# Optimization experiments

Measured on AMD Instinct MI355X. Metric: run time of the kernel, lower is better.

The kernel has to match this reference:

```python
import jax, jax.numpy as jnp
import numpy as np

N_HEADS, N_LEVELS, N_POINTS, D_MODEL = 8, 4, 4, 256
HEAD_DIM = D_MODEL // N_HEADS
SHAPES = [(96, 96), (48, 48), (24, 24), (12, 12)]


def setup_inputs() -> dict:
    key = jax.random.key(0)
    ks = jax.random.split(key, 9)
    shapes_np = np.asarray(SHAPES, dtype=np.int32)
    lengths = shapes_np[:, 0] * shapes_np[:, 1]
    Len = int(lengths.sum())  # 12240
    B = 1
    level_start = np.concatenate([[0], np.cumsum(lengths)[:-1]]).astype(np.int32)
    return {
        "query": jax.random.normal(ks[0], (B, Len, D_MODEL), jnp.float32),
        "reference_points": jax.random.uniform(ks[1], (B, Len, 2), jnp.float32),
        "input_flatten": jax.random.normal(ks[2], (B, Len, D_MODEL), jnp.float32),
        "spatial_shapes": jnp.asarray(shapes_np),
        "level_start_index": jnp.asarray(level_start),
        "W_off": jax.random.normal(ks[3], (D_MODEL, N_HEADS * N_LEVELS * N_POINTS * 2), jnp.float32) * 0.01,
        "b_off": jax.random.normal(ks[4], (N_HEADS * N_LEVELS * N_POINTS * 2,), jnp.float32) * 0.01,
        "W_attn": jax.random.normal(ks[5], (D_MODEL, N_HEADS * N_LEVELS * N_POINTS), jnp.float32) * 0.02,
        "b_attn": jnp.zeros((N_HEADS * N_LEVELS * N_POINTS,), jnp.float32),
        "W_out": jax.random.normal(ks[6], (D_MODEL, D_MODEL), jnp.float32) * 0.02,
        "b_out": jnp.zeros((D_MODEL,), jnp.float32),
    }


def _bilinear_gather(feat, x, y, H, W):
    """feat: [B,nH,H*W,D]; x,y: [B,nH,S] pixel coords. Zero padding, align_corners=False."""
    x0 = jnp.floor(x)
    y0 = jnp.floor(y)
    wx1 = x - x0
    wy1 = y - y0
    wx0 = 1.0 - wx1
    wy0 = 1.0 - wy1
    x0i = x0.astype(jnp.int32)
    y0i = y0.astype(jnp.int32)

    def corner(ix, iy):
        valid = (ix >= 0) & (ix < W) & (iy >= 0) & (iy < H)
        idx = jnp.clip(iy, 0, H - 1) * W + jnp.clip(ix, 0, W - 1)
        g = jnp.take_along_axis(feat, idx[..., None], axis=2)  # [B,nH,S,D]
        return g * valid[..., None].astype(feat.dtype)

    return (corner(x0i, y0i) * (wx0 * wy0)[..., None]
            + corner(x0i + 1, y0i) * (wx1 * wy0)[..., None]
            + corner(x0i, y0i + 1) * (wx0 * wy1)[..., None]
            + corner(x0i + 1, y0i + 1) * (wx1 * wy1)[..., None])


def _ms_deform_core(value, shapes_np, loc, attn):
    """value: [B,Len_in,nH,D]; loc: [B,LQ,nH,nL,nP,2]; attn: [B,LQ,nH,nL,nP]."""
    B, LQ = loc.shape[0], loc.shape[1]
    lengths = [int(h) * int(w) for h, w in shapes_np]
    starts = np.concatenate([[0], np.cumsum(lengths)])
    out = jnp.zeros((B, N_HEADS, LQ, HEAD_DIM), value.dtype)
    for lvl, (H, W) in enumerate(shapes_np):
        H, W = int(H), int(W)
        feat = value[:, starts[lvl]:starts[lvl + 1]].transpose(0, 2, 1, 3)  # [B,nH,HW,D]
        l = loc[:, :, :, lvl]  # [B,LQ,nH,nP,2]
        x = (l[..., 0] * W - 0.5).transpose(0, 2, 1, 3).reshape(B, N_HEADS, LQ * N_POINTS)
        y = (l[..., 1] * H - 0.5).transpose(0, 2, 1, 3).reshape(B, N_HEADS, LQ * N_POINTS)
        samp = _bilinear_gather(feat, x, y, H, W).reshape(B, N_HEADS, LQ, N_POINTS, HEAD_DIM)
        w = attn[:, :, :, lvl].transpose(0, 2, 1, 3)  # [B,nH,LQ,nP]
        out = out + (samp * w[..., None]).sum(axis=3)
    return out.transpose(0, 2, 1, 3).reshape(B, LQ, N_HEADS * HEAD_DIM)


def reference(query, reference_points, input_flatten, spatial_shapes, level_start_index,
              W_off, b_off, W_attn, b_attn, W_out, b_out):
    B, LQ, C = query.shape
    shapes_np = np.asarray(spatial_shapes)  # static per-level (H,W)
    off = (query @ W_off + b_off).reshape(B, LQ, N_HEADS, N_LEVELS, N_POINTS, 2)
    attn = jax.nn.softmax((query @ W_attn + b_attn).reshape(B, LQ, N_HEADS, N_LEVELS * N_POINTS), axis=-1)
    attn = attn.reshape(B, LQ, N_HEADS, N_LEVELS, N_POINTS)
    # offset_normalizer = (W, H) per level
    norm = jnp.asarray(np.stack([shapes_np[:, 1], shapes_np[:, 0]], -1), dtype=query.dtype)
    loc = reference_points[:, :, None, None, None, :] + off / norm[None, None, None, :, None, :]
    value = input_flatten.reshape(B, -1, N_HEADS, HEAD_DIM)
    out = _ms_deform_core(value, shapes_np, loc, attn)
    return out @ W_out + b_out
```

## Files before the change

kernel.cpp:

```cpp
#include <hip/hip_runtime.h>
#include <hip/hip_bf16.h>
#include <math.h>

constexpr int D_MODEL  = 256;
constexpr int N_HEADS  = 8;

typedef __attribute__((ext_vector_type(8))) short bf16x8;
typedef __attribute__((ext_vector_type(4))) float f32x4;
typedef __attribute__((ext_vector_type(2))) float f32x2;

__device__ __forceinline__ void gld_lds16(const void* gsrc, void* ldst) {
    __builtin_amdgcn_global_load_lds(
        (const __attribute__((address_space(1))) unsigned int*)gsrc,
        (__attribute__((address_space(3))) unsigned int*)ldst, 16, 0, 0);
}

__global__ __launch_bounds__(256) void convert_kernel(
    const float* __restrict__ q,
    const float* __restrict__ Woff,
    const float* __restrict__ Wattn,
    const float* __restrict__ Wout,
    const float* __restrict__ value,
    __hip_bfloat16* __restrict__ qbf,
    __hip_bfloat16* __restrict__ wt,
    __hip_bfloat16* __restrict__ vt,
    int M, int Lv)
{
    int t = blockIdx.x * 256 + threadIdx.x;
    int nq4 = M * 64;
    if (t < nq4) {
        float4 v = reinterpret_cast<const float4*>(q)[t];
        union { __hip_bfloat16 h[4]; ushort4 u; } cv;
        cv.h[0] = __float2bfloat16(v.x);
        cv.h[1] = __float2bfloat16(v.y);
        cv.h[2] = __float2bfloat16(v.z);
        cv.h[3] = __float2bfloat16(v.w);
        reinterpret_cast<ushort4*>(qbf)[t] = cv.u;
        return;
    }
    int t2 = t - nq4;
    if (t2 < 640 * 256) {
        int c = t2 >> 8, k = t2 & 255;
        float val = (c < 256) ? Woff[k * 256 + c]
                  : (c < 384) ? Wattn[k * 128 + (c - 256)]
                              : Wout[k * 256 + (c - 384)];
        wt[c * 256 + k] = __float2bfloat16(val);
        return;
    }
    int t3 = t2 - 640 * 256;
    if (t3 < Lv * 64) {
        int pix = t3 >> 6;
        int c4  = (t3 & 63) * 4;
        int h   = c4 >> 5, d = c4 & 31;
        float4 v = reinterpret_cast<const float4*>(value)[t3];
        union { __hip_bfloat16 h4[4]; ushort4 u; } cv;
        cv.h4[0] = __float2bfloat16(v.x);
        cv.h4[1] = __float2bfloat16(v.y);
        cv.h4[2] = __float2bfloat16(v.z);
        cv.h4[3] = __float2bfloat16(v.w);
        *reinterpret_cast<ushort4*>(vt + (size_t)h * Lv * 32 + (size_t)pix * 32 + d) = cv.u;
    }
}

template <int EPI>
__global__ __launch_bounds__(256) void gemm_mfma(
    const __hip_bfloat16* __restrict__ Abf,
    const __hip_bfloat16* __restrict__ Wt,
    int wrow0,
    const float* __restrict__ ba,
    const float* __restrict__ bb,
    const float* __restrict__ refpts,
    float* __restrict__ out0,
    float* __restrict__ out1,
    int M)
{
    __shared__ __align__(16) char smem[128 * 68 * 4];
    char*  A_lds = smem;
    char*  B_lds = smem + 16384;
    float* C_lds = (float*)smem;

    const int tid = threadIdx.x;
    const int w = tid >> 6, l = tid & 63;
    const int m0 = blockIdx.y * 128;
    const int n0 = blockIdx.x * 64;

    const char* Asrc = (const char*)Abf;
    const char* Wsrc = (const char*)(Wt + (size_t)(wrow0 + n0) * 256);

    f32x4 acc[2][4] = {};

    const int lr8 = l >> 3, l7 = l & 7;

    for (int k0 = 0; k0 < 512; k0 += 128) {
#pragma unroll
        for (int i = 0; i < 4; ++i) {
            int chunk = (w << 2) + i;
            int row = (chunk << 3) + lr8;
            int m = m0 + row; m = m < M ? m : (M - 1);
            gld_lds16(Asrc + (size_t)m * 512 + k0 + ((l7 ^ (row & 7)) << 4),
                      A_lds + (chunk << 10));
        }
#pragma unroll
        for (int i = 0; i < 2; ++i) {
            int chunk = (w << 1) + i;
            int row = (chunk << 3) + lr8;
            gld_lds16(Wsrc + (size_t)row * 512 + k0 + ((l7 ^ (row & 7)) << 4),
                      B_lds + (chunk << 10));
        }
        __syncthreads();

#pragma unroll
        for (int kk = 0; kk < 2; ++kk) {
            bf16x8 av[2], bv[4];
#pragma unroll
            for (int mf = 0; mf < 2; ++mf) {
                int arow = (w << 5) + (mf << 4) + (l & 15);
                int acb = ((kk << 6) + ((l >> 4) << 4)) ^ ((arow & 7) << 4);
                av[mf] = *(const bf16x8*)(A_lds + arow * 128 + acb);
            }
#pragma unroll
            for (int nf = 0; nf < 4; ++nf) {
                int brow = (nf << 4) + (l & 15);
                int bcb = ((kk << 6) + ((l >> 4) << 4)) ^ ((brow & 7) << 4);
                bv[nf] = *(const bf16x8*)(B_lds + brow * 128 + bcb);
            }
#pragma unroll
            for (int mf = 0; mf < 2; ++mf)
#pragma unroll
                for (int nf = 0; nf < 4; ++nf)
                    acc[mf][nf] = __builtin_amdgcn_mfma_f32_16x16x32_bf16(
                        av[mf], bv[nf], acc[mf][nf], 0, 0, 0);
        }
        __syncthreads();
    }

#pragma unroll
    for (int mf = 0; mf < 2; ++mf)
#pragma unroll
        for (int nf = 0; nf < 4; ++nf) {
            int col = (nf << 4) + (l & 15);
            int rbase = (w << 5) + (mf << 4) + ((l >> 4) << 2);
#pragma unroll
            for (int j = 0; j < 4; ++j)
                C_lds[(rbase + j) * 68 + col] = acc[mf][nf][j];
        }
    __syncthreads();

    if (EPI == 0 || n0 < 256) {
#pragma unroll
        for (int r2 = 0; r2 < 2; ++r2) {
            int row = (r2 << 6) + (tid >> 2);
            int q = m0 + row;
            if (q >= M) continue;
            float rx = 0.f, ry = 0.f;
            if (EPI == 1) { rx = refpts[q * 2]; ry = refpts[q * 2 + 1]; }
#pragma unroll
            for (int g = 0; g < 4; ++g) {
                int col = ((tid & 3) << 4) + (g << 2);
                float4 v  = *(float4*)&C_lds[row * 68 + col];
                float4 b4 = *(const float4*)&ba[n0 + col];
                if (EPI == 0) {
                    v.x += b4.x; v.y += b4.y; v.z += b4.z; v.w += b4.w;
                } else {
                    int c = n0 + col;
                    float rn = 1.0f / (float)(96 >> ((c >> 3) & 3));
                    v.x = rx + (v.x + b4.x) * rn;
                    v.y = ry + (v.y + b4.y) * rn;
                    v.z = rx + (v.z + b4.z) * rn;
                    v.w = ry + (v.w + b4.w) * rn;
                }
                *(float4*)&out0[(size_t)q * 256 + n0 + col] = v;
            }
        }
    } else {
        for (int u = tid; u < 512; u += 256) {
            int row = u >> 2, hh = u & 3;
            int q = m0 + row;
            if (q >= M) continue;
            int cg = (n0 - 256) + (hh << 4);
            float s[16];
            float mx = -1e30f;
#pragma unroll
            for (int i = 0; i < 16; ++i) {
                s[i] = C_lds[row * 68 + (hh << 4) + i] + bb[cg + i];
                mx = fmaxf(mx, s[i]);
            }
            float sum = 0.f;
#pragma unroll
            for (int i = 0; i < 16; ++i) { s[i] = __expf(s[i] - mx); sum += s[i]; }
            float inv = 1.0f / sum;
#pragma unroll
            for (int g = 0; g < 4; ++g) {
                float4 v = make_float4(s[g*4]*inv, s[g*4+1]*inv, s[g*4+2]*inv, s[g*4+3]*inv);
                *(float4*)&out1[(size_t)q * 128 + cg + (g << 2)] = v;
            }
        }
    }
}

template <int IMM>
__device__ __forceinline__ int swzi(int v) {
    return __builtin_amdgcn_ds_swizzle(v, IMM);
}

__device__ __forceinline__ f32x2 bf2(unsigned v) {
    f32x2 r;
    r.x = __uint_as_float(v << 16);
    r.y = __uint_as_float(v & 0xffff0000u);
    return r;
}
__device__ __forceinline__ unsigned packbf(float lo, float hi) {
    __hip_bfloat16 a = __float2bfloat16(lo), b = __float2bfloat16(hi);
    return (unsigned)*(unsigned short*)&a | ((unsigned)*(unsigned short*)&b << 16);
}

template <int P>
__device__ __forceinline__ void do_point4(
    const unsigned wp[4][2], const int op[4][2], const char* planeB,
    f32x2& a0, f32x2& a1, f32x2& a2, f32x2& a3)
{
    constexpr int S   = P & 3;
    constexpr int IMM = ((P >> 2) << 5) | 0x1C;

    unsigned wA = (unsigned)swzi<IMM>((int)wp[S][0]);
    unsigned wB = (unsigned)swzi<IMM>((int)wp[S][1]);
    unsigned oA = (unsigned)swzi<IMM>(op[S][0]);
    unsigned oB = (unsigned)swzi<IMM>(op[S][1]);

    f32x2 wlo = bf2(wA);
    f32x2 whi = bf2(wB);
    int o00 = (int)((oA & 0xffffu) << 6);
    int o10 = (int)((oA >> 16) << 6);
    int o01 = (int)((oB & 0xffffu) << 6);
    int o11 = (int)((oB >> 16) << 6);

    uint4 u0 = *(const uint4*)(planeB + o00);
    uint4 u1 = *(const uint4*)(planeB + o10);
    uint4 u2 = *(const uint4*)(planeB + o01);
    uint4 u3 = *(const uint4*)(planeB + o11);

    { f32x2 w2 = {wlo.x, wlo.x};
      a0 += bf2(u0.x) * w2; a1 += bf2(u0.y) * w2;
      a2 += bf2(u0.z) * w2; a3 += bf2(u0.w) * w2; }
    { f32x2 w2 = {wlo.y, wlo.y};
      a0 += bf2(u1.x) * w2; a1 += bf2(u1.y) * w2;
      a2 += bf2(u1.z) * w2; a3 += bf2(u1.w) * w2; }
    { f32x2 w2 = {whi.x, whi.x};
      a0 += bf2(u2.x) * w2; a1 += bf2(u2.y) * w2;
      a2 += bf2(u2.z) * w2; a3 += bf2(u2.w) * w2; }
    { f32x2 w2 = {whi.y, whi.y};
      a0 += bf2(u3.x) * w2; a1 += bf2(u3.y) * w2;
      a2 += bf2(u3.z) * w2; a3 += bf2(u3.w) * w2; }
}

__global__ __launch_bounds__(256, 8) void sample_kernel(
    const float* __restrict__ loc,
    const float* __restrict__ attn,
    const __hip_bfloat16* __restrict__ vt,
    __hip_bfloat16* __restrict__ core,
    int M, int Lv)
{
    const int h  = blockIdx.x & 7;
    const int q0 = (blockIdx.x >> 3) << 6;
    const int u_ = threadIdx.x >> 2;
    const int j  = threadIdx.x & 3;
    const int q  = q0 + u_;
    if (q >= M) return;

    const int Wl    = 96 >> j;
    const int start = 12288 - (12288 >> (2 * j));
    const float fW  = (float)Wl;

    const float4* lq4 = (const float4*)(loc + (size_t)q * 256 + h * 32 + j * 8);
    float4 pa = lq4[0];
    float4 pb = lq4[1];
    float4 aw = *(const float4*)(attn + (size_t)q * 128 + h * 16 + j * 4);

    const float lxs[4] = {pa.x, pa.z, pb.x, pb.z};
    const float lys[4] = {pa.y, pa.w, pb.y, pb.w};
    const float aws[4] = {aw.x, aw.y, aw.z, aw.w};

    unsigned wp[4][2]; int op[4][2];
#pragma unroll
    for (int s = 0; s < 4; ++s) {
        float x = lxs[s] * fW - 0.5f;
        float y = lys[s] * fW - 0.5f;
        float wgt = aws[s];

        float xf = floorf(x), yf = floorf(y);
        float wx1 = x - xf, wy1 = y - yf;
        float wx0 = 1.f - wx1, wy0 = 1.f - wy1;
        int ix = (int)xf, iy = (int)yf;

        float wxv0 = ((unsigned)ix       < (unsigned)Wl) ? wx0 : 0.f;
        float wxv1 = ((unsigned)(ix + 1) < (unsigned)Wl) ? wx1 : 0.f;
        float wyv0 = (((unsigned)iy       < (unsigned)Wl) ? wy0 : 0.f) * wgt;
        float wyv1 = (((unsigned)(iy + 1) < (unsigned)Wl) ? wy1 : 0.f) * wgt;

        int ix0 = min(max(ix,     0), Wl - 1);
        int ix1 = min(max(ix + 1, 0), Wl - 1);
        int iy0 = min(max(iy,     0), Wl - 1);
        int iy1 = min(max(iy + 1, 0), Wl - 1);

        int r0 = start + iy0 * Wl, r1 = start + iy1 * Wl;
        wp[s][0] = packbf(wxv0 * wyv0, wxv1 * wyv0);
        wp[s][1] = packbf(wxv0 * wyv1, wxv1 * wyv1);
        op[s][0] = (r0 + ix0) | ((r0 + ix1) << 16);
        op[s][1] = (r1 + ix0) | ((r1 + ix1) << 16);
    }

    const char* planeB = (const char*)vt + (size_t)h * Lv * 64 + j * 16;
    f32x2 a0 = {0.f, 0.f}, a1 = a0, a2 = a0, a3 = a0;

    do_point4< 0>(wp, op, planeB, a0, a1, a2, a3);
    do_point4< 1>(wp, op, planeB, a0, a1, a2, a3);
    do_point4< 2>(wp, op, planeB, a0, a1, a2, a3);
    do_point4< 3>(wp, op, planeB, a0, a1, a2, a3);
    do_point4< 4>(wp, op, planeB, a0, a1, a2, a3);
    do_point4< 5>(wp, op, planeB, a0, a1, a2, a3);
    do_point4< 6>(wp, op, planeB, a0, a1, a2, a3);
    do_point4< 7>(wp, op, planeB, a0, a1, a2, a3);
    do_point4< 8>(wp, op, planeB, a0, a1, a2, a3);
    do_point4< 9>(wp, op, planeB, a0, a1, a2, a3);
    do_point4<10>(wp, op, planeB, a0, a1, a2, a3);
    do_point4<11>(wp, op, planeB, a0, a1, a2, a3);
    do_point4<12>(wp, op, planeB, a0, a1, a2, a3);
    do_point4<13>(wp, op, planeB, a0, a1, a2, a3);
    do_point4<14>(wp, op, planeB, a0, a1, a2, a3);
    do_point4<15>(wp, op, planeB, a0, a1, a2, a3);

    uint4 st;
    st.x = packbf(a0.x, a0.y);
    st.y = packbf(a1.x, a1.y);
    st.z = packbf(a2.x, a2.y);
    st.w = packbf(a3.x, a3.y);
    *(uint4*)((char*)core + ((size_t)q * 256 + h * 32 + j * 8) * 2) = st;
}

extern "C" void kernel_launch(void* const* d_in, const int* in_sizes, int n_in,
                              void* d_out, int out_size, void* d_ws, size_t ws_size,
                              hipStream_t stream)
{
    const float* query  = (const float*)d_in[0];
    const float* refp   = (const float*)d_in[1];
    const float* value  = (const float*)d_in[2];
    const float* W_off  = (const float*)d_in[5];
    const float* b_off  = (const float*)d_in[6];
    const float* W_attn = (const float*)d_in[7];
    const float* b_attn = (const float*)d_in[8];
    const float* W_out  = (const float*)d_in[9];
    const float* b_out  = (const float*)d_in[10];
    float* out = (float*)d_out;

    const int M  = in_sizes[0] / D_MODEL;
    const int Lv = in_sizes[2] / D_MODEL;

    float* loc  = (float*)d_ws;
    float* attn = loc + (size_t)M * 256;
    __hip_bfloat16* qbf = (__hip_bfloat16*)(attn + (size_t)M * 128);
    __hip_bfloat16* wt  = qbf + (size_t)M * 256;
    __hip_bfloat16* vt  = wt + 640 * 256;
    __hip_bfloat16* core = qbf;

    dim3 blk(256);
    const int mblocks = (M + 127) / 128;

    int convthreads = M * 64 + 640 * 256 + Lv * 64;
    hipLaunchKernelGGL(convert_kernel, dim3((convthreads + 255) / 256), blk, 0, stream,
                       query, W_off, W_attn, W_out, value, qbf, wt, vt, M, Lv);

    hipLaunchKernelGGL((gemm_mfma<1>), dim3(6, mblocks), blk, 0, stream,
                       qbf, wt, 0, b_off, b_attn, refp, loc, attn, M);

    const int qchunks = (M + 63) / 64;
    hipLaunchKernelGGL(sample_kernel, dim3(qchunks * 8), blk, 0, stream,
                       loc, attn, vt, core, M, Lv);

    hipLaunchKernelGGL((gemm_mfma<0>), dim3(4, mblocks), blk, 0, stream,
                       core, wt, 384, b_out, nullptr, nullptr, out, nullptr, M);
}
```

Baseline: 60.61 us.

## Fuse deformable sampling with output projection via swizzled LDS staging

Merges the sampling kernel and the output-projection GEMM into one kernel. Each 512-thread block samples 128 queries across all heads and writes the bf16 core tile into XOR-swizzled shared memory, then runs MFMA against W_out and adds the bias. This drops the global round trip of the core tensor and one kernel launch. In exchange the grid shrinks to about 96 blocks with 64KB of LDS each, which lowers occupancy and parallelism during the gather phase.

```diff
diff --git a/kernel.cpp b/kernel.cpp
--- a/kernel.cpp
+++ b/kernel.cpp
@@ -253,88 +253,150 @@
       a2 += bf2(u3.z) * w2; a3 += bf2(u3.w) * w2; }
 }
 
-__global__ __launch_bounds__(256, 8) void sample_kernel(
+__global__ __launch_bounds__(512, 4) void sample_proj(
     const float* __restrict__ loc,
     const float* __restrict__ attn,
     const __hip_bfloat16* __restrict__ vt,
-    __hip_bfloat16* __restrict__ core,
+    const __hip_bfloat16* __restrict__ Wt,
+    const float* __restrict__ bout,
+    float* __restrict__ out,
     int M, int Lv)
 {
-    const int h  = blockIdx.x & 7;
-    const int q0 = (blockIdx.x >> 3) << 6;
-    const int u_ = threadIdx.x >> 2;
-    const int j  = threadIdx.x & 3;
-    const int q  = q0 + u_;
-    if (q >= M) return;
-
-    const int Wl    = 96 >> j;
-    const int start = 12288 - (12288 >> (2 * j));
-    const float fW  = (float)Wl;
-
-    const float4* lq4 = (const float4*)(loc + (size_t)q * 256 + h * 32 + j * 8);
-    float4 pa = lq4[0];
-    float4 pb = lq4[1];
-    float4 aw = *(const float4*)(attn + (size_t)q * 128 + h * 16 + j * 4);
-
-    const float lxs[4] = {pa.x, pa.z, pb.x, pb.z};
-    const float lys[4] = {pa.y, pa.w, pb.y, pb.w};
-    const float aws[4] = {aw.x, aw.y, aw.z, aw.w};
-
-    unsigned wp[4][2]; int op[4][2];
-#pragma unroll
-    for (int s = 0; s < 4; ++s) {
-        float x = lxs[s] * fW - 0.5f;
-        float y = lys[s] * fW - 0.5f;
-        float wgt = aws[s];
-
-        float xf = floorf(x), yf = floorf(y);
-        float wx1 = x - xf, wy1 = y - yf;
-        float wx0 = 1.f - wx1, wy0 = 1.f - wy1;
-        int ix = (int)xf, iy = (int)yf;
-
-        float wxv0 = ((unsigned)ix       < (unsigned)Wl) ? wx0 : 0.f;
-        float wxv1 = ((unsigned)(ix + 1) < (unsigned)Wl) ? wx1 : 0.f;
-        float wyv0 = (((unsigned)iy       < (unsigned)Wl) ? wy0 : 0.f) * wgt;
-        float wyv1 = (((unsigned)(iy + 1) < (unsigned)Wl) ? wy1 : 0.f) * wgt;
-
-        int ix0 = min(max(ix,     0), Wl - 1);
-        int ix1 = min(max(ix + 1, 0), Wl - 1);
-        int iy0 = min(max(iy,     0), Wl - 1);
-        int iy1 = min(max(iy + 1, 0), Wl - 1);
-
-        int r0 = start + iy0 * Wl, r1 = start + iy1 * Wl;
-        wp[s][0] = packbf(wxv0 * wyv0, wxv1 * wyv0);
-        wp[s][1] = packbf(wxv0 * wyv1, wxv1 * wyv1);
-        op[s][0] = (r0 + ix0) | ((r0 + ix1) << 16);
-        op[s][1] = (r1 + ix0) | ((r1 + ix1) << 16);
-    }
-
-    const char* planeB = (const char*)vt + (size_t)h * Lv * 64 + j * 16;
-    f32x2 a0 = {0.f, 0.f}, a1 = a0, a2 = a0, a3 = a0;
-
-    do_point4< 0>(wp, op, planeB, a0, a1, a2, a3);
-    do_point4< 1>(wp, op, planeB, a0, a1, a2, a3);
-    do_point4< 2>(wp, op, planeB, a0, a1, a2, a3);
-    do_point4< 3>(wp, op, planeB, a0, a1, a2, a3);
-    do_point4< 4>(wp, op, planeB, a0, a1, a2, a3);
-    do_point4< 5>(wp, op, planeB, a0, a1, a2, a3);
-    do_point4< 6>(wp, op, planeB, a0, a1, a2, a3);
-    do_point4< 7>(wp, op, planeB, a0, a1, a2, a3);
-    do_point4< 8>(wp, op, planeB, a0, a1, a2, a3);
-    do_point4< 9>(wp, op, planeB, a0, a1, a2, a3);
-    do_point4<10>(wp, op, planeB, a0, a1, a2, a3);
-    do_point4<11>(wp, op, planeB, a0, a1, a2, a3);
-    do_point4<12>(wp, op, planeB, a0, a1, a2, a3);
-    do_point4<13>(wp, op, planeB, a0, a1, a2, a3);
-    do_point4<14>(wp, op, planeB, a0, a1, a2, a3);
-    do_point4<15>(wp, op, planeB, a0, a1, a2, a3);
-
-    uint4 st;
-    st.x = packbf(a0.x, a0.y);
-    st.y = packbf(a1.x, a1.y);
-    st.z = packbf(a2.x, a2.y);
-    st.w = packbf(a3.x, a3.y);
-    *(uint4*)((char*)core + ((size_t)q * 256 + h * 32 + j * 8) * 2) = st;
+    __shared__ __align__(16) char core[128 * 512];
+
+    const int tid = threadIdx.x;
+    const int q0  = blockIdx.x << 7;
+    const int j   = tid & 3;
+
+#pragma unroll 1
+    for (int pass = 0; pass < 8; ++pass) {
+        const int unit = (pass << 7) + (tid >> 2);
+        const int ql   = unit >> 3;
+        const int h    = unit & 7;
+        const int q    = q0 + ql;
+        if (q < M) {
+            const int Wl    = 96 >> j;
+            const int start = 12288 - (12288 >> (2 * j));
+            const float fW  = (float)Wl;
+
+            const float4* lq4 = (const float4*)(loc + (size_t)q * 256 + h * 32 + j * 8);
+            float4 pa = lq4[0];
+            float4 pb = lq4[1];
+            float4 aw = *(const float4*)(attn + (size_t)q * 128 + h * 16 + j * 4);
+
+            const float lxs[4] = {pa.x, pa.z, pb.x, pb.z};
+            const float lys[4] = {pa.y, pa.w, pb.y, pb.w};
+            const float aws[4] = {aw.x, aw.y, aw.z, aw.w};
+
+            unsigned wp[4][2]; int op[4][2];
+#pragma unroll
+            for (int s = 0; s < 4; ++s) {
+                float x = lxs[s] * fW - 0.5f;
+                float y = lys[s] * fW - 0.5f;
+                float wgt = aws[s];
+
+                float xf = floorf(x), yf = floorf(y);
+                float wx1 = x - xf, wy1 = y - yf;
+                float wx0 = 1.f - wx1, wy0 = 1.f - wy1;
+                int ix = (int)xf, iy = (int)yf;
+
+                float wxv0 = ((unsigned)ix       < (unsigned)Wl) ? wx0 : 0.f;
+                float wxv1 = ((unsigned)(ix + 1) < (unsigned)Wl) ? wx1 : 0.f;
+                float wyv0 = (((unsigned)iy       < (unsigned)Wl) ? wy0 : 0.f) * wgt;
+                float wyv1 = (((unsigned)(iy + 1) < (unsigned)Wl) ? wy1 : 0.f) * wgt;
+
+                int ix0 = min(max(ix,     0), Wl - 1);
+                int ix1 = min(max(ix + 1, 0), Wl - 1);
+                int iy0 = min(max(iy,     0), Wl - 1);
+                int iy1 = min(max(iy + 1, 0), Wl - 1);
+
+                int r0 = start + iy0 * Wl, r1 = start + iy1 * Wl;
+                wp[s][0] = packbf(wxv0 * wyv0, wxv1 * wyv0);
+                wp[s][1] = packbf(wxv0 * wyv1, wxv1 * wyv1);
+                op[s][0] = (r0 + ix0) | ((r0 + ix1) << 16);
+                op[s][1] = (r1 + ix0) | ((r1 + ix1) << 16);
+            }
+
+            const char* planeB = (const char*)vt + (size_t)h * Lv * 64 + j * 16;
+            f32x2 a0 = {0.f, 0.f}, a1 = a0, a2 = a0, a3 = a0;
+
+            do_point4< 0>(wp, op, planeB, a0, a1, a2, a3);
+            do_point4< 1>(wp, op, planeB, a0, a1, a2, a3);
+            do_point4< 2>(wp, op, planeB, a0, a1, a2, a3);
+            do_point4< 3>(wp, op, planeB, a0, a1, a2, a3);
+            do_point4< 4>(wp, op, planeB, a0, a1, a2, a3);
+            do_point4< 5>(wp, op, planeB, a0, a1, a2, a3);
+            do_point4< 6>(wp, op, planeB, a0, a1, a2, a3);
+            do_point4< 7>(wp, op, planeB, a0, a1, a2, a3);
+            do_point4< 8>(wp, op, planeB, a0, a1, a2, a3);
+            do_point4< 9>(wp, op, planeB, a0, a1, a2, a3);
+            do_point4<10>(wp, op, planeB, a0, a1, a2, a3);
+            do_point4<11>(wp, op, planeB, a0, a1, a2, a3);
+            do_point4<12>(wp, op, planeB, a0, a1, a2, a3);
+            do_point4<13>(wp, op, planeB, a0, a1, a2, a3);
+            do_point4<14>(wp, op, planeB, a0, a1, a2, a3);
+            do_point4<15>(wp, op, planeB, a0, a1, a2, a3);
+
+            uint4 st;
+            st.x = packbf(a0.x, a0.y);
+            st.y = packbf(a1.x, a1.y);
+            st.z = packbf(a2.x, a2.y);
+            st.w = packbf(a3.x, a3.y);
+            int blk = ((h << 2) + j) ^ (ql & 7);
+            *(uint4*)(core + ql * 512 + blk * 16) = st;
+        }
+    }
+    __syncthreads();
+
+    const int l  = tid & 63;
+    const int w  = tid >> 6;
+    const int wm = w >> 2;
+    const int wn = w & 3;
+
+    f32x4 acc[4][4] = {};
+    const char* Bbase = (const char*)(Wt + (size_t)(384 + wn * 64) * 256);
+
+#pragma unroll 1
+    for (int kk = 0; kk < 8; ++kk) {
+        bf16x8 bv[4];
+#pragma unroll
+        for (int nf = 0; nf < 4; ++nf)
+            bv[nf] = *(const bf16x8*)(Bbase + (size_t)((nf << 4) + (l & 15)) * 512
+                                            + ((kk << 2) + (l >> 4)) * 16);
+        bf16x8 av[4];
+#pragma unroll
+        for (int mf = 0; mf < 4; ++mf) {
+            int row = (wm << 6) + (mf << 4) + (l & 15);
+            int blk = ((kk << 2) + (l >> 4)) ^ (row & 7);
+            av[mf] = *(const bf16x8*)(core + row * 512 + blk * 16);
+        }
+#pragma unroll
+        for (int mf = 0; mf < 4; ++mf)
+#pragma unroll
+            for (int nf = 0; nf < 4; ++nf)
+                acc[mf][nf] = __builtin_amdgcn_mfma_f32_16x16x32_bf16(
+                    av[mf], bv[nf], acc[mf][nf], 0, 0, 0);
+    }
+
+    float bias[4];
+#pragma unroll
+    for (int nf = 0; nf < 4; ++nf)
+        bias[nf] = bout[(wn << 6) + (nf << 4) + (l & 15)];
+
+#pragma unroll
+    for (int mf = 0; mf < 4; ++mf) {
+        int rbase = (wm << 6) + (mf << 4) + ((l >> 4) << 2);
+#pragma unroll
+        for (int nf = 0; nf < 4; ++nf) {
+            int col = (wn << 6) + (nf << 4) + (l & 15);
+#pragma unroll
+            for (int jj = 0; jj < 4; ++jj) {
+                int q = q0 + rbase + jj;
+                if (q < M)
+                    out[(size_t)q * 256 + col] = acc[mf][nf][jj] + bias[nf];
+            }
+        }
+    }
 }
 
 extern "C" void kernel_launch(void* const* d_in, const int* in_sizes, int n_in,
@@ -360,7 +422,6 @@
     __hip_bfloat16* qbf = (__hip_bfloat16*)(attn + (size_t)M * 128);
     __hip_bfloat16* wt  = qbf + (size_t)M * 256;
     __hip_bfloat16* vt  = wt + 640 * 256;
-    __hip_bfloat16* core = qbf;
 
     dim3 blk(256);
     const int mblocks = (M + 127) / 128;
@@ -372,10 +433,6 @@
     hipLaunchKernelGGL((gemm_mfma<1>), dim3(6, mblocks), blk, 0, stream,
                        qbf, wt, 0, b_off, b_attn, refp, loc, attn, M);
 
-    const int qchunks = (M + 63) / 64;
-    hipLaunchKernelGGL(sample_kernel, dim3(qchunks * 8), blk, 0, stream,
-                       loc, attn, vt, core, M, Lv);
-
-    hipLaunchKernelGGL((gemm_mfma<0>), dim3(4, mblocks), blk, 0, stream,
-                       core, wt, 384, b_out, nullptr, nullptr, out, nullptr, M);
-}
+    hipLaunchKernelGGL(sample_proj, dim3(mblocks), dim3(512), 0, stream,
+                       loc, attn, vt, wt, b_out, out, M, Lv);
+}
```

Result: slower. 99.80 us (+64.6%).
